# Optimization experiments

Measured on AMD Instinct MI355X. Metric: run time of the kernel, lower is better.

The kernel has to match this reference:

```python
import jax, jax.numpy as jnp
import numpy as np

B, C_IN, N = 16, 64, 40962          # icosphere level-6 node count
C_OUT = 32                           # out_feats; conv emits 7*C_OUT channels
NEW_N = 4 * N - 6                    # 163842
SEVEN_N = 7 * N                      # gather domain after reshape


def setup_inputs() -> dict:
    key = jax.random.key(0)
    k1, k2, k3, k4, k5 = jax.random.split(key, 5)
    x = jax.random.normal(k1, (B, C_IN, N), dtype=jnp.float32)
    W = jax.random.normal(k2, (7 * C_OUT, C_IN), dtype=jnp.float32) * (1.0 / np.sqrt(C_IN))
    b = jax.random.normal(k3, (7 * C_OUT,), dtype=jnp.float32) * 0.01
    top_idx = jax.random.randint(k4, (N,), 0, SEVEN_N, dtype=jnp.int64 if jax.config.jax_enable_x64 else jnp.int32)
    down_idx = jax.random.randint(k5, ((3 * N - 6) * 2,), 0, SEVEN_N, dtype=jnp.int64 if jax.config.jax_enable_x64 else jnp.int32)
    return {"x": x, "W": W, "b": b, "top_idx": top_idx, "down_idx": down_idx}


def reference(x, W, b, top_idx, down_idx):
    Bsz, _, n = x.shape
    c_out = W.shape[0] // 7
    # pointwise (kernel_size=1) Conv1d == GEMM over channels: [B,7*out,N]
    y = jnp.einsum('bcn,oc->bon', x, W) + b[None, :, None]
    # torch .view(B, out, 7N): row-major reshape, identical in jax
    y = y.reshape(Bsz, c_out, 7 * n)
    x1 = y[:, :, top_idx]                               # [B, out, N]
    x2 = y[:, :, down_idx].reshape(Bsz, c_out, -1, 2)   # [B, out, 3N-6, 2]
    out = jnp.concatenate([x1, x2.mean(axis=3)], axis=2)  # [B, out, 4N-6]
    return out
```

## Files before the change

### kernel.cpp

```cpp
#include <hip/hip_runtime.h>
#include <hip/hip_fp16.h>

#define BB     16
#define CIN    64
#define NN     40962
#define COUT   32
#define NEWN   (4*NN - 6)

typedef _Float16 h2v __attribute__((ext_vector_type(2)));

__device__ __forceinline__ float dot2h(int a, int b, float c) {
#if __has_builtin(__builtin_amdgcn_fdot2)
  return __builtin_amdgcn_fdot2(__builtin_bit_cast(h2v, a),
                                __builtin_bit_cast(h2v, b), c, false);
#else
  h2v av = __builtin_bit_cast(h2v, a);
  h2v bv = __builtin_bit_cast(h2v, b);
  c += (float)av.x * (float)bv.x;
  c += (float)av.y * (float)bv.y;
  return c;
#endif
}

__global__ __launch_bounds__(256) void k_transpose(const float* __restrict__ x,
                                                   __half* __restrict__ xT) {
  __shared__ float tile[64][65];
  const int b  = blockIdx.y;
  const int n0 = blockIdx.x * 64;
  const int lx = threadIdx.x & 63;
  const int ly = threadIdx.x >> 6;
  const float* xb = x + (size_t)b * CIN * NN;
  const int n = n0 + lx;
#pragma unroll
  for (int i = 0; i < 16; ++i) {
    int c = i * 4 + ly;
    tile[c][lx] = (n < NN) ? xb[(size_t)c * NN + n] : 0.f;
  }
  __syncthreads();
  __half* xTb = xT + (size_t)b * NN * CIN;
#pragma unroll
  for (int i = 0; i < 16; ++i) {
    int nl = i * 4 + ly;
    int nn = n0 + nl;
    if (nn < NN) xTb[(size_t)nn * CIN + lx] = __float2half(tile[lx][nl]);
  }
}

#define WP 36
#define TP (32*WP + 4)

__global__ __launch_bounds__(256) void k_upconv_f16(
    const __half* __restrict__ xT, const float* __restrict__ W,
    const float* __restrict__ bias, const int* __restrict__ top,
    const int* __restrict__ down, float* __restrict__ out) {
  __shared__ int   wl[7 * TP];
  __shared__ float bl[224];
  const int tid = threadIdx.x;

  for (int p = tid; p < 224 * 32; p += 256) {
    int o  = p >> 5;
    int cp = p & 31;
    h2v h;
    h.x = (_Float16)W[o * 64 + 2 * cp];
    h.y = (_Float16)W[o * 64 + 2 * cp + 1];
    wl[(o % 7) * TP + (o / 7) * WP + cp] = __builtin_bit_cast(int, h);
  }
  if (tid < 224) bl[tid] = bias[tid];
  __syncthreads();

  const int b = blockIdx.y;
  const int k = blockIdx.x * 256 + tid;

  int nit = 0, t0 = 0, t1 = 0, n0 = 0, n1 = 0;
  if (k < NEWN) {
    if (k < NN) {
      int j = top[k];
      t0 = j / NN; n0 = j - t0 * NN;
      nit = 1;
    } else {
      int kk = k - NN;
      int j1 = down[2 * kk];
      int j2 = down[2 * kk + 1];
      t0 = j1 / NN; n0 = j1 - t0 * NN;
      t1 = j2 / NN; n1 = j2 - t1 * NN;
      nit = 2;
    }
  }

  float acc[32];
#pragma unroll
  for (int i = 0; i < 32; ++i) acc[i] = 0.f;

  const __half* xTb = xT + (size_t)b * NN * CIN;
  for (int it = 0; it < nit; ++it) {
    const int t = it ? t1 : t0;
    const int n = it ? n1 : n0;
    const int4* col = (const int4*)(xTb + (size_t)n * CIN);
    const int base = t * TP;
#pragma unroll
    for (int hf = 0; hf < 2; ++hf) {
      int4 xv[4];
#pragma unroll
      for (int q = 0; q < 4; ++q) xv[q] = col[hf * 4 + q];
#pragma unroll
      for (int co = 0; co < 32; ++co) {
        float a = acc[co];
#pragma unroll
        for (int q = 0; q < 4; ++q) {
          int4 wv = *(const int4*)&wl[base + co * WP + (hf * 4 + q) * 4];
          a = dot2h(wv.x, xv[q].x, a);
          a = dot2h(wv.y, xv[q].y, a);
          a = dot2h(wv.z, xv[q].z, a);
          a = dot2h(wv.w, xv[q].w, a);
        }
        acc[co] = a;
      }
    }
  }

  if (k < NEWN) {
    float* ob = out + (size_t)b * COUT * NEWN + k;
    if (k < NN) {
#pragma unroll
      for (int co = 0; co < 32; ++co)
        ob[(size_t)co * NEWN] = acc[co] + bl[co * 7 + t0];
    } else {
#pragma unroll
      for (int co = 0; co < 32; ++co)
        ob[(size_t)co * NEWN] = 0.5f * (acc[co] + bl[co * 7 + t0] + bl[co * 7 + t1]);
    }
  }
}

#define WPB 68
#define TPB (32*WPB + 4)

__global__ __launch_bounds__(256) void k_upconv_f32(
    const float* __restrict__ x, const float* __restrict__ W,
    const float* __restrict__ bias, const int* __restrict__ top,
    const int* __restrict__ down, float* __restrict__ out) {
  __shared__ float wl[7 * TPB];
  __shared__ float bl[224];
  const int tid = threadIdx.x;
  for (int p = tid; p < 224 * 64; p += 256) {
    int o = p >> 6, c = p & 63;
    wl[(o % 7) * TPB + (o / 7) * WPB + c] = W[p];
  }
  if (tid < 224) bl[tid] = bias[tid];
  __syncthreads();

  const int b = blockIdx.y;
  const int k = blockIdx.x * 256 + tid;

  int nit = 0, t0 = 0, t1 = 0, n0 = 0, n1 = 0;
  if (k < NEWN) {
    if (k < NN) {
      int j = top[k];
      t0 = j / NN; n0 = j - t0 * NN; nit = 1;
    } else {
      int kk = k - NN;
      int j1 = down[2 * kk], j2 = down[2 * kk + 1];
      t0 = j1 / NN; n0 = j1 - t0 * NN;
      t1 = j2 / NN; n1 = j2 - t1 * NN;
      nit = 2;
    }
  }

  float acc[32];
#pragma unroll
  for (int i = 0; i < 32; ++i) acc[i] = 0.f;

  for (int it = 0; it < nit; ++it) {
    const int t = it ? t1 : t0;
    const int n = it ? n1 : n0;
    const float* col = x + (size_t)b * CIN * NN + n;
    const int base = t * TPB;
#pragma unroll
    for (int ch = 0; ch < 8; ++ch) {
      float xv[8];
#pragma unroll
      for (int q = 0; q < 8; ++q) xv[q] = col[(size_t)(ch * 8 + q) * NN];
#pragma unroll
      for (int co = 0; co < 32; ++co) {
        float a = acc[co];
        const float* wr = &wl[base + co * WPB + ch * 8];
        float4 w0 = *(const float4*)(wr);
        float4 w1 = *(const float4*)(wr + 4);
        a += w0.x * xv[0]; a += w0.y * xv[1]; a += w0.z * xv[2]; a += w0.w * xv[3];
        a += w1.x * xv[4]; a += w1.y * xv[5]; a += w1.z * xv[6]; a += w1.w * xv[7];
        acc[co] = a;
      }
    }
  }

  if (k < NEWN) {
    float* ob = out + (size_t)b * COUT * NEWN + k;
    if (k < NN) {
#pragma unroll
      for (int co = 0; co < 32; ++co)
        ob[(size_t)co * NEWN] = acc[co] + bl[co * 7 + t0];
    } else {
#pragma unroll
      for (int co = 0; co < 32; ++co)
        ob[(size_t)co * NEWN] = 0.5f * (acc[co] + bl[co * 7 + t0] + bl[co * 7 + t1]);
    }
  }
}

extern "C" void kernel_launch(void* const* d_in, const int* in_sizes, int n_in,
                              void* d_out, int out_size, void* d_ws, size_t ws_size,
                              hipStream_t stream) {
  const float* x    = (const float*)d_in[0];
  const float* W    = (const float*)d_in[1];
  const float* bias = (const float*)d_in[2];
  const int*   top  = (const int*)d_in[3];
  const int*   down = (const int*)d_in[4];
  float* out = (float*)d_out;

  const size_t xT_bytes = (size_t)BB * NN * CIN * sizeof(__half);
  if (ws_size >= xT_bytes) {
    __half* xT = (__half*)d_ws;
    k_transpose<<<dim3((NN + 63) / 64, BB), 256, 0, stream>>>(x, xT);
    k_upconv_f16<<<dim3((NEWN + 255) / 256, BB), 256, 0, stream>>>(xT, W, bias, top, down, out);
  } else {
    k_upconv_f32<<<dim3((NEWN + 255) / 256, BB), 256, 0, stream>>>(x, W, bias, top, down, out);
  }
}
```

Baseline: 716.9 us.

## Replace dot2 gather-conv with MFMA 32x32x16 over masked 7-tap K dimension

```diff
diff --git a/kernel.cpp b/kernel.cpp
--- a/kernel.cpp
+++ b/kernel.cpp
@@ -6,20 +6,20 @@
 #define NN     40962
 #define COUT   32
 #define NEWN   (4*NN - 6)
-
-typedef _Float16 h2v __attribute__((ext_vector_type(2)));
-
-__device__ __forceinline__ float dot2h(int a, int b, float c) {
-#if __has_builtin(__builtin_amdgcn_fdot2)
-  return __builtin_amdgcn_fdot2(__builtin_bit_cast(h2v, a),
-                                __builtin_bit_cast(h2v, b), c, false);
-#else
-  h2v av = __builtin_bit_cast(h2v, a);
-  h2v bv = __builtin_bit_cast(h2v, b);
-  c += (float)av.x * (float)bv.x;
-  c += (float)av.y * (float)bv.y;
-  return c;
-#endif
+#define GROUPS_PER_B ((NEWN + 31)/32)
+#define NGROUPS (BB * GROUPS_PER_B)
+
+typedef _Float16 f16x8  __attribute__((ext_vector_type(8)));
+typedef float    f32x16 __attribute__((ext_vector_type(16)));
+typedef _Float16 h2     __attribute__((ext_vector_type(2)));
+
+__device__ __forceinline__ int pk_add_h2(int a, int b) {
+  h2 r = __builtin_bit_cast(h2, a) + __builtin_bit_cast(h2, b);
+  return __builtin_bit_cast(int, r);
+}
+__device__ __forceinline__ int pack2(float lo, float hi) {
+  h2 r; r.x = (_Float16)lo; r.y = (_Float16)hi;
+  return __builtin_bit_cast(int, r);
 }
 
 __global__ __launch_bounds__(256) void k_transpose(const float* __restrict__ x,
@@ -46,88 +46,115 @@
   }
 }
 
-#define WP 36
-#define TP (32*WP + 4)
-
-__global__ __launch_bounds__(256) void k_upconv_f16(
+__global__ __launch_bounds__(256, 2) void k_upconv_mfma(
     const __half* __restrict__ xT, const float* __restrict__ W,
     const float* __restrict__ bias, const int* __restrict__ top,
     const int* __restrict__ down, float* __restrict__ out) {
-  __shared__ int   wl[7 * TP];
-  __shared__ float bl[224];
-  const int tid = threadIdx.x;
-
-  for (int p = tid; p < 224 * 32; p += 256) {
-    int o  = p >> 5;
-    int cp = p & 31;
-    h2v h;
-    h.x = (_Float16)W[o * 64 + 2 * cp];
-    h.y = (_Float16)W[o * 64 + 2 * cp + 1];
-    wl[(o % 7) * TP + (o / 7) * WP + cp] = __builtin_bit_cast(int, h);
-  }
-  if (tid < 224) bl[tid] = bias[tid];
-  __syncthreads();
-
-  const int b = blockIdx.y;
-  const int k = blockIdx.x * 256 + tid;
-
-  int nit = 0, t0 = 0, t1 = 0, n0 = 0, n1 = 0;
-  if (k < NEWN) {
-    if (k < NN) {
-      int j = top[k];
-      t0 = j / NN; n0 = j - t0 * NN;
-      nit = 1;
-    } else {
-      int kk = k - NN;
-      int j1 = down[2 * kk];
-      int j2 = down[2 * kk + 1];
-      t0 = j1 / NN; n0 = j1 - t0 * NN;
-      t1 = j2 / NN; n1 = j2 - t1 * NN;
-      nit = 2;
-    }
-  }
-
-  float acc[32];
-#pragma unroll
-  for (int i = 0; i < 32; ++i) acc[i] = 0.f;
-
-  const __half* xTb = xT + (size_t)b * NN * CIN;
-  for (int it = 0; it < nit; ++it) {
-    const int t = it ? t1 : t0;
-    const int n = it ? n1 : n0;
-    const int4* col = (const int4*)(xTb + (size_t)n * CIN);
-    const int base = t * TP;
-#pragma unroll
-    for (int hf = 0; hf < 2; ++hf) {
-      int4 xv[4];
-#pragma unroll
-      for (int q = 0; q < 4; ++q) xv[q] = col[hf * 4 + q];
-#pragma unroll
-      for (int co = 0; co < 32; ++co) {
-        float a = acc[co];
-#pragma unroll
-        for (int q = 0; q < 4; ++q) {
-          int4 wv = *(const int4*)&wl[base + co * WP + (hf * 4 + q) * 4];
-          a = dot2h(wv.x, xv[q].x, a);
-          a = dot2h(wv.y, xv[q].y, a);
-          a = dot2h(wv.z, xv[q].z, a);
-          a = dot2h(wv.w, xv[q].w, a);
-        }
-        acc[co] = a;
-      }
-    }
-  }
-
-  if (k < NEWN) {
-    float* ob = out + (size_t)b * COUT * NEWN + k;
-    if (k < NN) {
-#pragma unroll
-      for (int co = 0; co < 32; ++co)
-        ob[(size_t)co * NEWN] = acc[co] + bl[co * 7 + t0];
-    } else {
-#pragma unroll
-      for (int co = 0; co < 32; ++co)
-        ob[(size_t)co * NEWN] = 0.5f * (acc[co] + bl[co * 7 + t0] + bl[co * 7 + t1]);
+  const int lane = threadIdx.x & 63;
+  const int co   = lane & 31;
+  const int h    = lane >> 5;
+  const int waveInBlock = threadIdx.x >> 6;
+  const int gwave = blockIdx.x * (blockDim.x >> 6) + waveInBlock;
+  const int nwaves = gridDim.x * (blockDim.x >> 6);
+
+  int4 Af[29];
+#pragma unroll
+  for (int s = 0; s < 28; ++s) {
+    const int t  = s >> 2;
+    const int c0 = 16 * (s & 3) + 8 * h;
+    const float* wr = W + (co * 7 + t) * 64 + c0;
+    float4 wa = *(const float4*)wr;
+    float4 wb = *(const float4*)(wr + 4);
+    Af[s].x = pack2(0.5f * wa.x, 0.5f * wa.y);
+    Af[s].y = pack2(0.5f * wa.z, 0.5f * wa.w);
+    Af[s].z = pack2(0.5f * wb.x, 0.5f * wb.y);
+    Af[s].w = pack2(0.5f * wb.z, 0.5f * wb.w);
+  }
+  {
+    int4 ab = {0, 0, 0, 0};
+    if (h == 0) {
+      float bv[8];
+#pragma unroll
+      for (int tau = 0; tau < 7; ++tau) bv[tau] = 0.5f * bias[co * 7 + tau];
+      bv[7] = 0.f;
+      ab.x = pack2(bv[0], bv[1]);
+      ab.y = pack2(bv[2], bv[3]);
+      ab.z = pack2(bv[4], bv[5]);
+      ab.w = pack2(bv[6], bv[7]);
+    }
+    Af[28] = ab;
+  }
+
+  for (int gid = gwave; gid < NGROUPS; gid += nwaves) {
+    const int b = gid / GROUPS_PER_B;
+    const int g = gid - b * GROUPS_PER_B;
+    const int k = g * 32 + co;
+    const bool valid = (k < NEWN);
+
+    int j1 = 0, j2 = 0;
+    if (valid) {
+      if (k < NN) { j1 = top[k]; j2 = j1; }
+      else {
+        const int kk = k - NN;
+        j1 = down[2 * kk];
+        j2 = down[2 * kk + 1];
+      }
+    }
+    const int t0 = j1 / NN, n0 = j1 - t0 * NN;
+    const int t1 = j2 / NN, n1 = j2 - t1 * NN;
+
+    const __half* xTb = xT + (size_t)b * NN * CIN;
+    const int4* base0 = (const int4*)(xTb + (size_t)n0 * CIN);
+    const int4* base1 = (const int4*)(xTb + (size_t)n1 * CIN);
+    int4 col0[4], col1[4];
+#pragma unroll
+    for (int q = 0; q < 4; ++q) col0[q] = base0[2 * q + h];
+#pragma unroll
+    for (int q = 0; q < 4; ++q) col1[q] = base1[2 * q + h];
+
+    f32x16 acc;
+#pragma unroll
+    for (int i = 0; i < 16; ++i) acc[i] = 0.f;
+
+#pragma unroll
+    for (int s = 0; s < 28; ++s) {
+      const int t = s >> 2, q = s & 3;
+      const bool m0 = (t0 == t), m1 = (t1 == t);
+      int4 bb;
+      bb.x = pk_add_h2(m0 ? col0[q].x : 0, m1 ? col1[q].x : 0);
+      bb.y = pk_add_h2(m0 ? col0[q].y : 0, m1 ? col1[q].y : 0);
+      bb.z = pk_add_h2(m0 ? col0[q].z : 0, m1 ? col1[q].z : 0);
+      bb.w = pk_add_h2(m0 ? col0[q].w : 0, m1 ? col1[q].w : 0);
+      acc = __builtin_amdgcn_mfma_f32_32x32x16_f16(
+          __builtin_bit_cast(f16x8, Af[s]), __builtin_bit_cast(f16x8, bb), acc, 0, 0, 0);
+    }
+
+    {
+      int4 bsel = {0, 0, 0, 0};
+      if (h == 0) {
+        float c0f = (float)((t0 == 0) + (t1 == 0));
+        float c1f = (float)((t0 == 1) + (t1 == 1));
+        float c2f = (float)((t0 == 2) + (t1 == 2));
+        float c3f = (float)((t0 == 3) + (t1 == 3));
+        float c4f = (float)((t0 == 4) + (t1 == 4));
+        float c5f = (float)((t0 == 5) + (t1 == 5));
+        float c6f = (float)((t0 == 6) + (t1 == 6));
+        bsel.x = pack2(c0f, c1f);
+        bsel.y = pack2(c2f, c3f);
+        bsel.z = pack2(c4f, c5f);
+        bsel.w = pack2(c6f, 0.f);
+      }
+      acc = __builtin_amdgcn_mfma_f32_32x32x16_f16(
+          __builtin_bit_cast(f16x8, Af[28]), __builtin_bit_cast(f16x8, bsel), acc, 0, 0, 0);
+    }
+
+    if (valid) {
+      float* ob = out + (size_t)b * COUT * NEWN + k;
+#pragma unroll
+      for (int r = 0; r < 16; ++r) {
+        const int corow = (r & 3) + 8 * (r >> 2) + 4 * h;
+        ob[(size_t)corow * NEWN] = acc[r];
+      }
     }
   }
 }
@@ -221,7 +248,7 @@
   if (ws_size >= xT_bytes) {
     __half* xT = (__half*)d_ws;
     k_transpose<<<dim3((NN + 63) / 64, BB), 256, 0, stream>>>(x, xT);
-    k_upconv_f16<<<dim3((NEWN + 255) / 256, BB), 256, 0, stream>>>(xT, W, bias, top, down, out);
+    k_upconv_mfma<<<dim3(512), 256, 0, stream>>>(xT, W, bias, top, down, out);
   } else {
     k_upconv_f32<<<dim3((NEWN + 255) / 256, BB), 256, 0, stream>>>(x, W, bias, top, down, out);
   }
```

Result: faster. 614.6 us (-14.3%).
